# Kernel tuning notes

Measured on AMD Instinct MI355X. Metric: run time of the kernel, lower is better.

The kernel has to match this reference:

```python
import jax, jax.numpy as jnp
import numpy as np
from jax.scipy.special import digamma

N, D, K = 32768, 64, 64


def setup_inputs() -> dict:
    key = jax.random.key(0)
    k1, k2, k3, k4, k5, k6, k7 = jax.random.split(key, 7)
    X = jax.random.normal(k1, (N, D), dtype=jnp.float32)
    means = jax.random.normal(k2, (K, D), dtype=jnp.float32)
    # Upper-triangular precision Cholesky factors with strictly positive diagonal
    # (matches solve_triangular(L, I).T from the torch code).
    off = jnp.triu(jax.random.normal(k3, (K, D, D), dtype=jnp.float32) * 0.05, 1)
    diag = jnp.exp(jax.random.normal(k4, (K, D), dtype=jnp.float32) * 0.1)
    precisions_chol = off + jax.vmap(jnp.diag)(diag)
    weight_concentration = jax.random.uniform(k5, (2, K), dtype=jnp.float32, minval=0.5, maxval=5.0)
    # degrees_of_freedom must be > D - 1 so digamma args stay positive
    degrees_of_freedom = jnp.float32(D) + jax.random.uniform(k6, (K,), dtype=jnp.float32, minval=1.0, maxval=50.0)
    mean_precision = jax.random.uniform(k7, (K,), dtype=jnp.float32, minval=0.5, maxval=10.0)
    return {"X": X, "means": means, "precisions_chol": precisions_chol,
            "weight_concentration": weight_concentration,
            "degrees_of_freedom": degrees_of_freedom, "mean_precision": mean_precision}


def _weighted_log_prob(X, means, precisions_chol, weight_concentration,
                       degrees_of_freedom, mean_precision):
    n_features = X.shape[1]
    # log|prec_chol_k| = sum of log of diagonal entries
    log_det = jnp.sum(jnp.log(jnp.diagonal(precisions_chol, axis1=1, axis2=2)), axis=1)  # [K]
    # whitened residuals: y[n,k,:] = X[n] @ P_k - mu_k @ P_k
    XP = jnp.einsum('nd,kde->nke', X, precisions_chol)            # [N,K,D]
    muP = jnp.einsum('kd,kde->ke', means, precisions_chol)        # [K,D]
    sq = jnp.sum(jnp.square(XP - muP[None]), axis=-1)             # [N,K]
    log2pi = jnp.log(jnp.float32(2.0 * np.pi))
    log_gauss = -0.5 * (n_features * log2pi + sq) + log_det[None]
    # Bayesian corrections
    log_gauss = log_gauss - 0.5 * n_features * jnp.log(degrees_of_freedom)[None]
    i = jnp.arange(n_features, dtype=jnp.float32)
    log_lambda = n_features * jnp.log(jnp.float32(2.0)) + jnp.sum(
        digamma(0.5 * (degrees_of_freedom[None, :] - i[:, None])), axis=0)  # [K]
    log_prob = log_gauss + 0.5 * (log_lambda - n_features / mean_precision)[None]
    # stick-breaking log weights (dirichlet_process)
    a, b = weight_concentration[0], weight_concentration[1]
    dsum = digamma(a + b)
    log_w = digamma(a) - dsum + jnp.concatenate(
        [jnp.zeros((1,), dtype=X.dtype), jnp.cumsum(digamma(b) - dsum)[:-1]])
    return log_prob + log_w[None]


def reference(X, means, precisions_chol, weight_concentration,
              degrees_of_freedom, mean_precision):
    wlp = _weighted_log_prob(X, means, precisions_chol, weight_concentration,
                             degrees_of_freedom, mean_precision)
    return jnp.argmax(wlp, axis=1)
```

## Files before the change

kernel.cpp:

```cpp
#include <hip/hip_runtime.h>
#include <math.h>

#define N_ROWS 32768
#define DIM 64
#define KCOMP 64
#define KSPLIT 8
#define KLOCAL 8
#define THREADS 256
#define PREP_THREADS 256
#define RT 4
#define ROWS_PER_WAVE 64
#define ROWS_PER_BLOCK 256
#define ROWGROUPS (N_ROWS / ROWS_PER_BLOCK)

#define PT_K_BYTES 16384

#define LOG2PI_D 1.8378770664093454836

typedef _Float16 f16x8 __attribute__((ext_vector_type(8)));
typedef float f32x4 __attribute__((ext_vector_type(4)));

#define AS1 __attribute__((address_space(1)))
#define AS3 __attribute__((address_space(3)))

__device__ __forceinline__ void async_copy16(const char* g, char* l) {
  __builtin_amdgcn_global_load_lds((const AS1 unsigned int*)g,
                                   (AS3 unsigned int*)l, 16, 0, 0);
}

__device__ __forceinline__ double digamma_d(double x) {
  double r = 0.0;
  while (x < 6.0) { r -= 1.0 / x; x += 1.0; }
  double inv = 1.0 / x;
  double inv2 = inv * inv;
  double s = log(x) - 0.5 * inv
      - inv2 * (1.0/12.0 - inv2 * (1.0/120.0 - inv2 * (1.0/252.0
      - inv2 * (1.0/240.0 - inv2 * (1.0/132.0)))));
  return r + s;
}

__global__ void prep1_kernel(const float* __restrict__ means,
                             const float* __restrict__ P,
                             const float* __restrict__ wc,
                             const float* __restrict__ dof,
                             const float* __restrict__ mp,
                             char*   __restrict__ Pt,
                             float*  __restrict__ muP,
                             double* __restrict__ t_arr,
                             double* __restrict__ g_arr,
                             double* __restrict__ pc_arr)
{
  __shared__ float lds[DIM][DIM + 1];
  const int k = blockIdx.x;
  const int t = threadIdx.x;
  const float* Pk = P + k * DIM * DIM;

  for (int i = t; i < DIM * DIM; i += PREP_THREADS)
    lds[i >> 6][i & 63] = Pk[i];
  __syncthreads();

  char* dst = Pt + (size_t)k * PT_K_BYTES;
#pragma unroll
  for (int cc = 0; cc < 4; ++cc) {
    int cid  = cc * PREP_THREADS + t;
    int blk  = cid >> 7;
    int sel  = (cid >> 6) & 1;
    int lane = cid & 63;
    int et = blk >> 1, c = blk & 1;
    int m = lane & 15, q = lane >> 4;
    int e = et * 16 + m;
    int d0 = c * 32 + q * 8;
    f16x8 o;
#pragma unroll
    for (int j = 0; j < 8; ++j) {
      float v = lds[d0 + j][e];
      _Float16 h = (_Float16)v;
      o[j] = sel ? (_Float16)(v - (float)h) : h;
    }
    *(f16x8*)(dst + cid * 16) = o;
  }

  if (t < 64) {
    const int i = t;
    const float* mk = means + k * DIM;
    float acc = 0.f;
#pragma unroll 8
    for (int d = 0; d < DIM; ++d) acc = fmaf(mk[d], lds[d][i], acc);
    muP[k * DIM + i] = acc;

    double dofk = (double)dof[k];
    double s1 = digamma_d(0.5 * (dofk - (double)i));
    double s2 = log((double)lds[i][i]);
#pragma unroll
    for (int off = 32; off > 0; off >>= 1) {
      s1 += __shfl_down(s1, off);
      s2 += __shfl_down(s2, off);
    }
    if (i == 0) {
      double ak = (double)wc[k], bk = (double)wc[KCOMP + k];
      double dgab = digamma_d(ak + bk);
      double log_lambda = (double)DIM * log(2.0) + s1;
      double pc = s2
                - 0.5 * (double)DIM * LOG2PI_D
                - 0.5 * (double)DIM * log(dofk)
                + 0.5 * (log_lambda - (double)DIM / (double)mp[k]);
      t_arr[k] = digamma_d(bk) - dgab;
      g_arr[k] = digamma_d(ak) - dgab;
      pc_arr[k] = pc;
    }
  }
}

__global__ __launch_bounds__(THREADS, 4) void main_kernel(
    const float* __restrict__ X,
    const char*  __restrict__ Pt,
    const float* __restrict__ muP,
    const double* __restrict__ t_arr,
    const double* __restrict__ g_arr,
    const double* __restrict__ pc_arr,
    unsigned long long* __restrict__ packed,
    int* __restrict__ cnt,
    int* __restrict__ out)
{
  __shared__ uint4 bbuf[2][PT_K_BYTES / 16];
  __shared__ float cvec_lds[KCOMP];
  __shared__ float mup_lds[KLOCAL * DIM];
  __shared__ int is_last;

  const int tid  = threadIdx.x;
  const int wave = tid >> 6;
  const int lane = tid & 63;
  const int m    = lane & 15;
  const int q    = lane >> 4;
  const int ks   = blockIdx.y;
  const int rowbase = blockIdx.x * ROWS_PER_BLOCK + wave * ROWS_PER_WAVE;
  const int k0   = ks * KLOCAL;

  {
    const char* src = Pt + (size_t)k0 * PT_K_BYTES;
#pragma unroll
    for (int i = 0; i < 4; ++i) {
      const int g = wave * 4 + i;
      async_copy16(src + (g << 10) + (lane << 4),
                   (char*)&bbuf[0][g << 6]);
    }
  }

  if (tid < 64) {
    double t = t_arr[tid];
    double s = t;
#pragma unroll
    for (int off = 1; off < 64; off <<= 1) {
      double v = __shfl_up(s, off);
      if (tid >= off) s += v;
    }
    cvec_lds[tid] = (float)(pc_arr[tid] + g_arr[tid] + (s - t));
  }
  for (int i = tid; i < KLOCAL * DIM; i += THREADS)
    mup_lds[i] = muP[ks * KLOCAL * DIM + i];

  f16x8 ahi[RT][2], alo[RT][2];
#pragma unroll
  for (int rt = 0; rt < RT; ++rt) {
    int row = rowbase + rt * 16 + m;
    const float* xp = X + row * DIM;
#pragma unroll
    for (int c = 0; c < 2; ++c) {
      const float4* xq4 = (const float4*)(xp + c * 32 + q * 8);
      float4 v0 = xq4[0], v1 = xq4[1];
      float xv[8] = {v0.x, v0.y, v0.z, v0.w, v1.x, v1.y, v1.z, v1.w};
      f16x8 h, l;
#pragma unroll
      for (int j = 0; j < 8; ++j) {
        _Float16 hv = (_Float16)xv[j];
        h[j] = hv;
        l[j] = (_Float16)(xv[j] - (float)hv);
      }
      ahi[rt][c] = h;
      alo[rt][c] = l;
    }
  }

  __syncthreads();

  float best = -INFINITY;
  int   bidx = 0;
  const bool b0 = (m & 1), b1 = (m & 2), b2 = (m & 4), b3 = (m & 8);

  for (int ki = 0; ki < KLOCAL; ++ki) {
    const int k = k0 + ki;
    const int p = ki & 1;

    if (ki + 1 < KLOCAL) {
      const char* src = Pt + (size_t)(k + 1) * PT_K_BYTES;
#pragma unroll
      for (int i = 0; i < 4; ++i) {
        const int g = wave * 4 + i;
        async_copy16(src + (g << 10) + (lane << 4),
                     (char*)&bbuf[1 - p][g << 6]);
      }
    }

    const char* lb = (const char*)bbuf[p];
    const float ck = cvec_lds[k];
    float sq[16];
#pragma unroll
    for (int i = 0; i < 16; ++i) sq[i] = 0.f;

#pragma unroll
    for (int et = 0; et < 4; ++et) {
      const float mval = -mup_lds[(ki << 6) + et * 16 + m];
      f32x4 acc[RT];
#pragma unroll
      for (int rt = 0; rt < RT; ++rt)
#pragma unroll
        for (int r = 0; r < 4; ++r) acc[rt][r] = mval;

#pragma unroll
      for (int c = 0; c < 2; ++c) {
        const char* bp = lb + ((et * 2 + c) << 11) + (lane << 4);
        f16x8 bh = *(const f16x8*)bp;
        f16x8 bl = *(const f16x8*)(bp + 1024);
#pragma unroll
        for (int rt = 0; rt < RT; ++rt) {
          acc[rt] = __builtin_amdgcn_mfma_f32_16x16x32_f16(ahi[rt][c], bh, acc[rt], 0, 0, 0);
          acc[rt] = __builtin_amdgcn_mfma_f32_16x16x32_f16(ahi[rt][c], bl, acc[rt], 0, 0, 0);
          acc[rt] = __builtin_amdgcn_mfma_f32_16x16x32_f16(alo[rt][c], bh, acc[rt], 0, 0, 0);
        }
      }
#pragma unroll
      for (int rt = 0; rt < RT; ++rt)
#pragma unroll
        for (int r = 0; r < 4; ++r)
          sq[rt * 4 + r] = fmaf(acc[rt][r], acc[rt][r], sq[rt * 4 + r]);
    }

    float v8[8];
#pragma unroll
    for (int pp = 0; pp < 8; ++pp) {
      float keep = b0 ? sq[2*pp+1] : sq[2*pp];
      float send = b0 ? sq[2*pp]   : sq[2*pp+1];
      v8[pp] = keep + __shfl_xor(send, 1);
    }
    float v4[4];
#pragma unroll
    for (int pp = 0; pp < 4; ++pp) {
      float keep = b1 ? v8[2*pp+1] : v8[2*pp];
      float send = b1 ? v8[2*pp]   : v8[2*pp+1];
      v4[pp] = keep + __shfl_xor(send, 2);
    }
    float v2[2];
#pragma unroll
    for (int pp = 0; pp < 2; ++pp) {
      float keep = b2 ? v4[2*pp+1] : v4[2*pp];
      float send = b2 ? v4[2*pp]   : v4[2*pp+1];
      v2[pp] = keep + __shfl_xor(send, 4);
    }
    float keep = b3 ? v2[1] : v2[0];
    float send = b3 ? v2[0] : v2[1];
    float z = keep + __shfl_xor(send, 8);

    float wv = fmaf(-0.5f, z, ck);
    if (wv > best || (wv == best && k < bidx)) { best = wv; bidx = k; }

    __syncthreads();
  }

  {
    int row = rowbase + (m >> 2) * 16 + q * 4 + (m & 3);
    unsigned int b = __float_as_uint(best);
    unsigned int u = (b & 0x80000000u) ? ~b : (b | 0x80000000u);
    unsigned long long pkd = ((unsigned long long)u << 32)
                           | (unsigned long long)(63 - bidx);
    atomicMax(&packed[row], pkd);
  }
  __builtin_amdgcn_s_waitcnt(0);
  __syncthreads();
  if (tid == 0) {
    int old = atomicAdd(&cnt[blockIdx.x], 1);
    is_last = (old == KSPLIT - 1);
  }
  __syncthreads();
  if (is_last) {
    int n = blockIdx.x * ROWS_PER_BLOCK + tid;
    unsigned long long pv = __hip_atomic_load(&packed[n], __ATOMIC_RELAXED,
                                              __HIP_MEMORY_SCOPE_AGENT);
    out[n] = 63 - (int)(pv & 63ull);
  }
}

extern "C" void kernel_launch(void* const* d_in, const int* in_sizes, int n_in,
                              void* d_out, int out_size, void* d_ws, size_t ws_size,
                              hipStream_t stream) {
  const float* X     = (const float*)d_in[0];
  const float* means = (const float*)d_in[1];
  const float* P     = (const float*)d_in[2];
  const float* wc    = (const float*)d_in[3];
  const float* dof   = (const float*)d_in[4];
  const float* mp    = (const float*)d_in[5];
  int* out = (int*)d_out;

  char* wsb = (char*)d_ws;
  float*  muP    = (float*)(wsb);
  double* t_arr  = (double*)(wsb + 16640);
  double* g_arr  = (double*)(wsb + 17152);
  double* pc_arr = (double*)(wsb + 17664);
  int*    cnt    = (int*)(wsb + 20480);
  unsigned long long* packed = (unsigned long long*)(wsb + 24576);
  char*   Pt     = wsb + 294912;

  hipMemsetAsync(wsb + 20480, 0, 286720 - 20480, stream);

  prep1_kernel<<<KCOMP, PREP_THREADS, 0, stream>>>(means, P, wc, dof, mp, Pt,
                                                   muP, t_arr, g_arr, pc_arr);

  dim3 grid(ROWGROUPS, KSPLIT);
  main_kernel<<<grid, THREADS, 0, stream>>>(X, Pt, muP, t_arr, g_arr, pc_arr,
                                            packed, cnt, out);
}
```

Baseline: 115.3 us.

## Overlap per-component shuffle reduction with next component's MFMAs; fold memset into prep

Splits the cross-lane butterfly reduction of the previous component's squared distances into stages interleaved with the four MFMA tiles of the next component, with a tail reduction after the loop. This lets shuffle latency hide behind matrix work instead of serialising each iteration. It also removes the separate hipMemsetAsync by zeroing the packed argmax buffer and counters inside the prep kernel, saving one launch. The cost is more live registers (sqp and the partial vectors), which may pressure occupancy.

```diff
diff --git a/kernel.cpp b/kernel.cpp
--- a/kernel.cpp
+++ b/kernel.cpp
@@ -48,12 +48,18 @@
                              float*  __restrict__ muP,
                              double* __restrict__ t_arr,
                              double* __restrict__ g_arr,
-                             double* __restrict__ pc_arr)
+                             double* __restrict__ pc_arr,
+                             uint4*  __restrict__ packed4,
+                             uint4*  __restrict__ cnt4)
 {
   __shared__ float lds[DIM][DIM + 1];
   const int k = blockIdx.x;
   const int t = threadIdx.x;
   const float* Pk = P + k * DIM * DIM;
+
+  const uint4 z4 = {0u, 0u, 0u, 0u};
+  packed4[k * PREP_THREADS + t] = z4;
+  if (k == 0 && t < 64) cnt4[t] = z4;
 
   for (int i = t; i < DIM * DIM; i += PREP_THREADS)
     lds[i >> 6][i & 63] = Pk[i];
@@ -187,6 +193,11 @@
   int   bidx = 0;
   const bool b0 = (m & 1), b1 = (m & 2), b2 = (m & 4), b3 = (m & 8);
 
+  float sqp[16];
+  float fv8[8], fv4[4], fv2[2];
+  float ckp = 0.f;
+  int   kprev = 0;
+
   for (int ki = 0; ki < KLOCAL; ++ki) {
     const int k = k0 + ki;
     const int p = ki & 1;
@@ -215,6 +226,37 @@
       for (int rt = 0; rt < RT; ++rt)
 #pragma unroll
         for (int r = 0; r < 4; ++r) acc[rt][r] = mval;
+
+      if (ki > 0) {
+        if (et == 0) {
+#pragma unroll
+          for (int pp = 0; pp < 8; ++pp) {
+            float keep = b0 ? sqp[2*pp+1] : sqp[2*pp];
+            float send = b0 ? sqp[2*pp]   : sqp[2*pp+1];
+            fv8[pp] = keep + __shfl_xor(send, 1);
+          }
+        } else if (et == 1) {
+#pragma unroll
+          for (int pp = 0; pp < 4; ++pp) {
+            float keep = b1 ? fv8[2*pp+1] : fv8[2*pp];
+            float send = b1 ? fv8[2*pp]   : fv8[2*pp+1];
+            fv4[pp] = keep + __shfl_xor(send, 2);
+          }
+        } else if (et == 2) {
+#pragma unroll
+          for (int pp = 0; pp < 2; ++pp) {
+            float keep = b2 ? fv4[2*pp+1] : fv4[2*pp];
+            float send = b2 ? fv4[2*pp]   : fv4[2*pp+1];
+            fv2[pp] = keep + __shfl_xor(send, 4);
+          }
+        } else {
+          float keep = b3 ? fv2[1] : fv2[0];
+          float send = b3 ? fv2[0] : fv2[1];
+          float z = keep + __shfl_xor(send, 8);
+          float wv = fmaf(-0.5f, z, ckp);
+          if (wv > best || (wv == best && kprev < bidx)) { best = wv; bidx = kprev; }
+        }
+      }
 
 #pragma unroll
       for (int c = 0; c < 2; ++c) {
@@ -235,35 +277,38 @@
           sq[rt * 4 + r] = fmaf(acc[rt][r], acc[rt][r], sq[rt * 4 + r]);
     }
 
-    float v8[8];
+#pragma unroll
+    for (int i = 0; i < 16; ++i) sqp[i] = sq[i];
+    ckp = ck;
+    kprev = k;
+
+    __syncthreads();
+  }
+
+  {
 #pragma unroll
     for (int pp = 0; pp < 8; ++pp) {
-      float keep = b0 ? sq[2*pp+1] : sq[2*pp];
-      float send = b0 ? sq[2*pp]   : sq[2*pp+1];
-      v8[pp] = keep + __shfl_xor(send, 1);
-    }
-    float v4[4];
+      float keep = b0 ? sqp[2*pp+1] : sqp[2*pp];
+      float send = b0 ? sqp[2*pp]   : sqp[2*pp+1];
+      fv8[pp] = keep + __shfl_xor(send, 1);
+    }
 #pragma unroll
     for (int pp = 0; pp < 4; ++pp) {
-      float keep = b1 ? v8[2*pp+1] : v8[2*pp];
-      float send = b1 ? v8[2*pp]   : v8[2*pp+1];
-      v4[pp] = keep + __shfl_xor(send, 2);
-    }
-    float v2[2];
+      float keep = b1 ? fv8[2*pp+1] : fv8[2*pp];
+      float send = b1 ? fv8[2*pp]   : fv8[2*pp+1];
+      fv4[pp] = keep + __shfl_xor(send, 2);
+    }
 #pragma unroll
     for (int pp = 0; pp < 2; ++pp) {
-      float keep = b2 ? v4[2*pp+1] : v4[2*pp];
-      float send = b2 ? v4[2*pp]   : v4[2*pp+1];
-      v2[pp] = keep + __shfl_xor(send, 4);
-    }
-    float keep = b3 ? v2[1] : v2[0];
-    float send = b3 ? v2[0] : v2[1];
+      float keep = b2 ? fv4[2*pp+1] : fv4[2*pp];
+      float send = b2 ? fv4[2*pp]   : fv4[2*pp+1];
+      fv2[pp] = keep + __shfl_xor(send, 4);
+    }
+    float keep = b3 ? fv2[1] : fv2[0];
+    float send = b3 ? fv2[0] : fv2[1];
     float z = keep + __shfl_xor(send, 8);
-
-    float wv = fmaf(-0.5f, z, ck);
-    if (wv > best || (wv == best && k < bidx)) { best = wv; bidx = k; }
-
-    __syncthreads();
+    float wv = fmaf(-0.5f, z, ckp);
+    if (wv > best || (wv == best && kprev < bidx)) { best = wv; bidx = kprev; }
   }
 
   {
@@ -309,10 +354,9 @@
   unsigned long long* packed = (unsigned long long*)(wsb + 24576);
   char*   Pt     = wsb + 294912;
 
-  hipMemsetAsync(wsb + 20480, 0, 286720 - 20480, stream);
-
   prep1_kernel<<<KCOMP, PREP_THREADS, 0, stream>>>(means, P, wc, dof, mp, Pt,
-                                                   muP, t_arr, g_arr, pc_arr);
+                                                   muP, t_arr, g_arr, pc_arr,
+                                                   (uint4*)packed, (uint4*)cnt);
 
   dim3 grid(ROWGROUPS, KSPLIT);
   main_kernel<<<grid, THREADS, 0, stream>>>(X, Pt, muP, t_arr, g_arr, pc_arr,
```

Result: slower. 266.9 us (+131.4%).
